# Optimization experiments

Measured on AMD Instinct MI355X. Metric: run time of the kernel, lower is better.

## Reference

```python
import jax, jax.numpy as jnp
import numpy as np

N_ATOMS = 65536
N_PAIRS = 16777216
N_MOL = 2048
RADIUS = 5.0
ECONV = 14.399645  # eV*Angstrom Coulomb constant


def setup_inputs() -> dict:
    key = jax.random.key(0)
    k1, k2, k3, k4, k5 = jax.random.split(key, 5)
    charges = jax.random.normal(k1, (N_ATOMS, 1), dtype=jnp.float32)
    # distances in (0.5, 1.2*RADIUS): some pairs beyond the screening radius
    pair_dist = jax.random.uniform(k2, (N_PAIRS,), dtype=jnp.float32,
                                   minval=0.5, maxval=1.2 * RADIUS)
    pair_first = jax.random.randint(k3, (N_PAIRS,), 0, N_ATOMS)
    pair_second = jax.random.randint(k4, (N_PAIRS,), 0, N_ATOMS)
    mol_index = jnp.sort(jax.random.randint(k5, (N_ATOMS,), 0, N_MOL))
    return {
        "charges": charges,
        "pair_dist": pair_dist,
        "pair_first": pair_first,
        "pair_second": pair_second,
        "mol_index": mol_index,
        "n_molecules": N_MOL,
    }


def _cosine_screening(pair_dist, radius):
    # smooth cosine screening: 1 at r=0, 0 at r=radius
    return 0.5 * (1.0 + jnp.cos(jnp.pi * pair_dist / radius))


def reference(charges, pair_dist, pair_first, pair_second, mol_index, n_molecules):
    # gather charges for each pair, screened Coulomb per pair  [n_pairs, 1]
    qi = charges[pair_first, 0]
    qj = charges[pair_second, 0]
    base = qi * qj / pair_dist
    scr = _cosine_screening(pair_dist, RADIUS)
    scr = jnp.where(pair_dist < RADIUS, scr, jnp.zeros_like(scr))
    coulomb_pairs = base * scr  # [n_pairs]
    # MolPairSummer: scatter pairs into molecules via mol_index[pair_first]
    pair_mol = mol_index[pair_first]
    coulomb_molecule = jax.ops.segment_sum(coulomb_pairs, pair_mol,
                                           num_segments=n_molecules)
    coulomb_molecule = 0.5 * ECONV * coulomb_molecule
    return coulomb_molecule[:, None]  # [n_molecules, 1]
```

## Files before the change

### kernel.cpp

```cpp
#include <hip/hip_runtime.h>
#include <hip/hip_fp16.h>


#define NMOL_MAX 2048
constexpr float RADIUS = 5.0f;
constexpr float ECONV  = 14.399645f;

typedef float f4 __attribute__((ext_vector_type(4)));
typedef int   i4 __attribute__((ext_vector_type(4)));

__global__ __launch_bounds__(256) void prep_tabs(const float* __restrict__ q,
                                                 const int* __restrict__ mol,
                                                 __half* __restrict__ q16,
                                                 ushort* __restrict__ mol16, int n) {
    int i = blockIdx.x * 256 + threadIdx.x;
    if (i < n) {
        q16[i] = __float2half(q[i]);
        mol16[i] = (ushort)mol[i];
    }
}

__global__ __launch_bounds__(1024) void pair_bins(const f4* __restrict__ dist4,
                                                  const i4* __restrict__ first4,
                                                  const i4* __restrict__ second4,
                                                  const ushort* __restrict__ mol16,
                                                  const __half* __restrict__ q16,
                                                  float* __restrict__ partial,
                                                  int nvec, int n_atoms, int n_mol) {
    extern __shared__ char smem[];
    __half* qt  = (__half*)smem;
    float* bins = (float*)(smem + (size_t)n_atoms * 2);

    {
        const f4* src = (const f4*)q16;
        f4* dst = (f4*)qt;
        int nv = n_atoms >> 3;
        for (int i = threadIdx.x; i < nv; i += 1024) dst[i] = src[i];
        for (int m = threadIdx.x; m < n_mol; m += 1024) bins[m] = 0.0f;
    }
    __syncthreads();

    const float c = 3.14159265358979323846f / RADIUS;
    const int stride = gridDim.x * 1024;
    for (int v = blockIdx.x * 1024 + threadIdx.x; v < nvec; v += stride) {
        const f4 d4 = __builtin_nontemporal_load(dist4 + v);
        const i4 fi = __builtin_nontemporal_load(first4 + v);
        const i4 si = __builtin_nontemporal_load(second4 + v);
        ushort mk[4];
#pragma unroll
        for (int k = 0; k < 4; ++k) mk[k] = mol16[fi[k]];
        float qi[4], qj[4];
#pragma unroll
        for (int k = 0; k < 4; ++k) {
            qi[k] = __half2float(qt[fi[k]]);
            qj[k] = __half2float(qt[si[k]]);
        }
#pragma unroll
        for (int k = 0; k < 4; ++k) {
            const float d = d4[k];
            const float scr = (d < RADIUS) ? 0.5f * (1.0f + __cosf(d * c)) : 0.0f;
            const float val = qi[k] * qj[k] * __fdividef(scr, d);
            atomicAdd(&bins[mk[k]], val);
        }
    }
    __syncthreads();
    float* p = partial + (size_t)blockIdx.x * n_mol;
    for (int m = threadIdx.x; m < n_mol; m += 1024) p[m] = bins[m];
}

__global__ __launch_bounds__(256) void reduce_full(const float* __restrict__ partial,
                                                   float* __restrict__ out,
                                                   int nblk, int n_mol) {
    int m = blockIdx.x * 256 + threadIdx.x;
    if (m >= n_mol) return;
    float s0 = 0.f, s1 = 0.f, s2 = 0.f, s3 = 0.f;
    int b = 0;
    for (; b + 4 <= nblk; b += 4) {
        s0 += partial[(size_t)(b + 0) * n_mol + m];
        s1 += partial[(size_t)(b + 1) * n_mol + m];
        s2 += partial[(size_t)(b + 2) * n_mol + m];
        s3 += partial[(size_t)(b + 3) * n_mol + m];
    }
    for (; b < nblk; ++b) s0 += partial[(size_t)b * n_mol + m];
    out[m] = 0.5f * ECONV * ((s0 + s1) + (s2 + s3));
}

extern "C" void kernel_launch(void* const* d_in, const int* in_sizes, int n_in,
                              void* d_out, int out_size, void* d_ws, size_t ws_size,
                              hipStream_t stream) {
    const float* charges     = (const float*)d_in[0];
    const float* pair_dist   = (const float*)d_in[1];
    const int*   pair_first  = (const int*)d_in[2];
    const int*   pair_second = (const int*)d_in[3];
    const int*   mol_index   = (const int*)d_in[4];
    const int n_atoms = in_sizes[0];
    const int n_pairs = in_sizes[1];
    const int n_mol   = out_size;
    const int nvec    = n_pairs >> 2;

    char* w = (char*)d_ws;
    __half* q16  = (__half*)w;
    size_t off1 = ((size_t)n_atoms * 2 + 255) & ~(size_t)255;
    ushort* mol16 = (ushort*)(w + off1);
    size_t off2 = off1 + (((size_t)n_atoms * 2 + 255) & ~(size_t)255);
    float* partial = (float*)(w + off2);

    const int nblk = 256;
    const size_t smem_bytes = (size_t)n_atoms * 2 + (size_t)n_mol * 4;
    hipFuncSetAttribute((const void*)pair_bins,
                        hipFuncAttributeMaxDynamicSharedMemorySize,
                        (int)smem_bytes);

    prep_tabs<<<(n_atoms + 255) / 256, 256, 0, stream>>>(charges, mol_index, q16, mol16, n_atoms);
    pair_bins<<<nblk, 1024, smem_bytes, stream>>>((const f4*)pair_dist,
                                                  (const i4*)pair_first,
                                                  (const i4*)pair_second,
                                                  mol16, q16, partial,
                                                  nvec, n_atoms, n_mol);
    reduce_full<<<(n_mol + 255) / 256, 256, 0, stream>>>(partial, (float*)d_out, nblk, n_mol);
}
```

Measured before the change: 272.0 us.

## Encode sorted mol_index as LDS bitmask chunks and software-pipeline pair loads

Replaces the global ushort mol16 gather with a compact per-32-atom record (segment-change bitmask plus base id) held in LDS, so the molecule id comes from a popcount instead of a random global load. The fp16 charge conversion moves into each block's LDS fill, and the pair loop prefetches two iterations ahead to hide streaming latency. The encoding relies on mol_index being sorted with steps of at most one between neighbours, and each block now redoes the fp32-to-half conversion and uses more LDS and registers.

```diff
diff --git a/kernel.cpp b/kernel.cpp
--- a/kernel.cpp
+++ b/kernel.cpp
@@ -2,67 +2,95 @@
 #include <hip/hip_fp16.h>
 
 
-#define NMOL_MAX 2048
 constexpr float RADIUS = 5.0f;
 constexpr float ECONV  = 14.399645f;
 
 typedef float f4 __attribute__((ext_vector_type(4)));
 typedef int   i4 __attribute__((ext_vector_type(4)));
 
-__global__ __launch_bounds__(256) void prep_tabs(const float* __restrict__ q,
-                                                 const int* __restrict__ mol,
-                                                 __half* __restrict__ q16,
-                                                 ushort* __restrict__ mol16, int n) {
-    int i = blockIdx.x * 256 + threadIdx.x;
-    if (i < n) {
-        q16[i] = __float2half(q[i]);
-        mol16[i] = (ushort)mol[i];
+__global__ __launch_bounds__(256) void prep_mol(const int* __restrict__ mol,
+                                                uint2* __restrict__ rec, int nchunk) {
+    int c = blockIdx.x * 256 + threadIdx.x;
+    if (c >= nchunk) return;
+    const int* p = mol + c * 32;
+    int base = p[0];
+    unsigned mask = 0;
+    int prev = base;
+#pragma unroll
+    for (int i = 1; i < 32; ++i) {
+        int m = p[i];
+        if (m != prev) mask |= (1u << i);
+        prev = m;
     }
+    rec[c] = make_uint2(mask, (unsigned)base);
 }
 
 __global__ __launch_bounds__(1024) void pair_bins(const f4* __restrict__ dist4,
                                                   const i4* __restrict__ first4,
                                                   const i4* __restrict__ second4,
-                                                  const ushort* __restrict__ mol16,
-                                                  const __half* __restrict__ q16,
+                                                  const float* __restrict__ qf32,
+                                                  const uint2* __restrict__ molrec_g,
                                                   float* __restrict__ partial,
                                                   int nvec, int n_atoms, int n_mol) {
     extern __shared__ char smem[];
-    __half* qt  = (__half*)smem;
-    float* bins = (float*)(smem + (size_t)n_atoms * 2);
+    float* bins = (float*)smem;
+    uint2* mrec = (uint2*)(smem + (size_t)n_mol * 4);
+    const int nchunk = n_atoms >> 5;
+    __half* qt = (__half*)(smem + (size_t)n_mol * 4 + (size_t)nchunk * 8);
 
+    for (int m = threadIdx.x; m < n_mol; m += 1024) bins[m] = 0.0f;
+    for (int c = threadIdx.x; c < nchunk; c += 1024) mrec[c] = molrec_g[c];
     {
-        const f4* src = (const f4*)q16;
-        f4* dst = (f4*)qt;
-        int nv = n_atoms >> 3;
-        for (int i = threadIdx.x; i < nv; i += 1024) dst[i] = src[i];
-        for (int m = threadIdx.x; m < n_mol; m += 1024) bins[m] = 0.0f;
+        const f4* src = (const f4*)qf32;
+        int nv = n_atoms >> 2;
+        for (int i = threadIdx.x; i < nv; i += 1024) {
+            f4 q = src[i];
+            __half2* dst = (__half2*)(qt + (size_t)i * 4);
+            dst[0] = __floats2half2_rn(q.x, q.y);
+            dst[1] = __floats2half2_rn(q.z, q.w);
+        }
     }
     __syncthreads();
 
-    const float c = 3.14159265358979323846f / RADIUS;
+    const float c_rad = 3.14159265358979323846f / RADIUS;
     const int stride = gridDim.x * 1024;
-    for (int v = blockIdx.x * 1024 + threadIdx.x; v < nvec; v += stride) {
-        const f4 d4 = __builtin_nontemporal_load(dist4 + v);
-        const i4 fi = __builtin_nontemporal_load(first4 + v);
-        const i4 si = __builtin_nontemporal_load(second4 + v);
-        ushort mk[4];
-#pragma unroll
-        for (int k = 0; k < 4; ++k) mk[k] = mol16[fi[k]];
-        float qi[4], qj[4];
+    const int v0 = blockIdx.x * 1024 + threadIdx.x;
+
+    int vc = v0;
+    bool pc_ = vc < nvec; int ac = pc_ ? vc : 0;
+    f4 dc = __builtin_nontemporal_load(dist4 + ac);
+    i4 fc = __builtin_nontemporal_load(first4 + ac);
+    i4 sc = __builtin_nontemporal_load(second4 + ac);
+    int vn = v0 + stride;
+    bool pn_ = vn < nvec; int an = pn_ ? vn : 0;
+    f4 dn = __builtin_nontemporal_load(dist4 + an);
+    i4 fn = __builtin_nontemporal_load(first4 + an);
+    i4 sn = __builtin_nontemporal_load(second4 + an);
+
+    for (int vt = v0 + 2 * stride; pc_; vt += stride) {
+        bool pt_ = vt < nvec; int at = pt_ ? vt : 0;
+        f4 dt = __builtin_nontemporal_load(dist4 + at);
+        i4 ft = __builtin_nontemporal_load(first4 + at);
+        i4 st = __builtin_nontemporal_load(second4 + at);
+
 #pragma unroll
         for (int k = 0; k < 4; ++k) {
-            qi[k] = __half2float(qt[fi[k]]);
-            qj[k] = __half2float(qt[si[k]]);
+            const int f = fc[k];
+            const int s = sc[k];
+            const uint2 r = mrec[f >> 5];
+            const int mi = (int)r.y + __popc(r.x & ((2u << (f & 31)) - 1u));
+            const float qi = __half2float(qt[f]);
+            const float qj = __half2float(qt[s]);
+            const float d  = dc[k];
+            const float scr = (d < RADIUS) ? 0.5f * (1.0f + __cosf(d * c_rad)) : 0.0f;
+            const float val = qi * qj * __fdividef(scr, d);
+            atomicAdd(&bins[mi], val);
         }
-#pragma unroll
-        for (int k = 0; k < 4; ++k) {
-            const float d = d4[k];
-            const float scr = (d < RADIUS) ? 0.5f * (1.0f + __cosf(d * c)) : 0.0f;
-            const float val = qi[k] * qj[k] * __fdividef(scr, d);
-            atomicAdd(&bins[mk[k]], val);
-        }
+
+        dc = dn; fc = fn; sc = sn; pc_ = pn_;
+        dn = dt; fn = ft; sn = st; pn_ = pt_;
     }
+
     __syncthreads();
     float* p = partial + (size_t)blockIdx.x * n_mol;
     for (int m = threadIdx.x; m < n_mol; m += 1024) p[m] = bins[m];
@@ -97,25 +125,23 @@
     const int n_pairs = in_sizes[1];
     const int n_mol   = out_size;
     const int nvec    = n_pairs >> 2;
+    const int nchunk  = n_atoms >> 5;
 
-    char* w = (char*)d_ws;
-    __half* q16  = (__half*)w;
-    size_t off1 = ((size_t)n_atoms * 2 + 255) & ~(size_t)255;
-    ushort* mol16 = (ushort*)(w + off1);
-    size_t off2 = off1 + (((size_t)n_atoms * 2 + 255) & ~(size_t)255);
-    float* partial = (float*)(w + off2);
+    uint2* molrec = (uint2*)d_ws;
+    size_t off = ((size_t)nchunk * 8 + 255) & ~(size_t)255;
+    float* partial = (float*)((char*)d_ws + off);
 
     const int nblk = 256;
-    const size_t smem_bytes = (size_t)n_atoms * 2 + (size_t)n_mol * 4;
+    const size_t smem_bytes = (size_t)n_mol * 4 + (size_t)nchunk * 8 + (size_t)n_atoms * 2;
     hipFuncSetAttribute((const void*)pair_bins,
                         hipFuncAttributeMaxDynamicSharedMemorySize,
                         (int)smem_bytes);
 
-    prep_tabs<<<(n_atoms + 255) / 256, 256, 0, stream>>>(charges, mol_index, q16, mol16, n_atoms);
+    prep_mol<<<(nchunk + 255) / 256, 256, 0, stream>>>(mol_index, molrec, nchunk);
     pair_bins<<<nblk, 1024, smem_bytes, stream>>>((const f4*)pair_dist,
                                                   (const i4*)pair_first,
                                                   (const i4*)pair_second,
-                                                  mol16, q16, partial,
+                                                  charges, molrec, partial,
                                                   nvec, n_atoms, n_mol);
     reduce_full<<<(n_mol + 255) / 256, 256, 0, stream>>>(partial, (float*)d_out, nblk, n_mol);
 }
```

Measured after the change: 281.3 us. 3.4% more time.
